# Kernel tuning notes

Measured on AMD Instinct MI355X. Metric: run time of the kernel, lower is better.

Reference implementation:

```python
import jax, jax.numpy as jnp
import numpy as np

EMBEDDING_DIM = 10
CONTEXT_SIZE_1 = 1
CONTEXT_SIZE_2 = 3
VOCAB = 50000
N = 1_000_000
NUM_NUMERIC = 16


def setup_inputs() -> dict:
    key = jax.random.key(0)
    ks = jax.random.split(key, 9)
    text_1 = jax.random.randint(ks[0], (N,), 0, VOCAB)
    text_2 = jax.random.randint(ks[1], (N,), 0, VOCAB)
    numeric_features = jax.random.normal(ks[2], (N, NUM_NUMERIC), dtype=jnp.float32)
    emb_table_1 = jax.random.normal(ks[3], (VOCAB, EMBEDDING_DIM), dtype=jnp.float32)
    emb_table_2 = jax.random.normal(ks[4], (VOCAB, EMBEDDING_DIM), dtype=jnp.float32)
    d_in = 2 * EMBEDDING_DIM + NUM_NUMERIC
    W1 = jax.random.normal(ks[5], (d_in, 128), dtype=jnp.float32) / np.sqrt(d_in)
    b1 = jnp.zeros((128,), dtype=jnp.float32)
    W2 = jax.random.normal(ks[6], (128, 1), dtype=jnp.float32) / np.sqrt(128.0)
    b2 = jnp.zeros((1,), dtype=jnp.float32)
    return {
        "text_1": text_1,
        "text_2": text_2,
        "numeric_features": numeric_features,
        "emb_table_1": emb_table_1,
        "emb_table_2": emb_table_2,
        "W1": W1,
        "b1": b1,
        "W2": W2,
        "b2": b2,
    }


def _contextual_embedding(ids, table, context_size):
    # mean of embeddings over window [i-cs, i+cs], clipped at sequence edges
    n = ids.shape[0]
    emb = table[ids]  # [N, D] gather
    # prefix sums with leading zero row: S[j] = sum(emb[0:j])
    S = jnp.concatenate([jnp.zeros((1, emb.shape[1]), emb.dtype),
                         jnp.cumsum(emb, axis=0)], axis=0)
    pos = jnp.arange(n)
    lo = jnp.maximum(pos - context_size, 0)
    hi = jnp.minimum(pos + context_size + 1, n)
    wsum = S[hi] - S[lo]                       # [N, D]
    count = (hi - lo).astype(emb.dtype)[:, None]
    return wsum / count


def reference(text_1, text_2, numeric_features, emb_table_1, emb_table_2, W1, b1, W2, b2):
    embed_1 = _contextual_embedding(text_1, emb_table_1, CONTEXT_SIZE_1)  # [N, 10]
    embed_2 = _contextual_embedding(text_2, emb_table_2, CONTEXT_SIZE_2)  # [N, 10]
    combined = jnp.concatenate([embed_1, embed_2, numeric_features], axis=1)
    h = jax.nn.relu(combined @ W1 + b1)
    out = h @ W2 + b2
    return jax.nn.sigmoid(out)  # [N, 1]
```

## Files before the change

### kernel.cpp

```cpp
#include <hip/hip_runtime.h>
#include <hip/hip_bf16.h>

#define EMB 10
#define DIN 36
#define HID 128
#define BM  128

typedef __attribute__((ext_vector_type(8))) short short8;
typedef __attribute__((ext_vector_type(4))) float f32x4;

__device__ __forceinline__ short bf16_hi(float v) {
  __hip_bfloat16 h = __float2bfloat16(v);
  return *reinterpret_cast<short*>(&h);
}
__device__ __forceinline__ float bf16_to_f(short s) {
  __hip_bfloat16 h = *reinterpret_cast<__hip_bfloat16*>(&s);
  return __bfloat162float(h);
}

__global__ void prep_kernel(const float* __restrict__ W1, const float* __restrict__ b1,
                            short* __restrict__ Bpack) {
  int b = blockIdx.x;
  int term = b >> 4;
  int ct   = (b >> 1) & 7;
  int ks   = b & 1;
  int l = threadIdx.x;
  int col = ct * 16 + (l & 15);
  int kb  = ks * 32 + (l >> 4) * 8;
  short8 o;
#pragma unroll
  for (int e = 0; e < 8; ++e) {
    int k = kb + e;
    float v = 0.0f;
    if (k < DIN)       v = W1[k * HID + col];
    else if (k == DIN) v = b1[col];
    short hb = bf16_hi(v);
    o[e] = (term == 0) ? hb : bf16_hi(v - bf16_to_f(hb));
  }
  *(short8*)(Bpack + (size_t)(((term * 8 + ct) * 2 + ks) * 64 + l) * 8) = o;
}

__global__ __launch_bounds__(256, 3)
void fused_kernel(const int* __restrict__ t1, const int* __restrict__ t2,
                  const float* __restrict__ numf,
                  const float* __restrict__ tab1, const float* __restrict__ tab2,
                  const short* __restrict__ Bpack,
                  const float* __restrict__ W2, const float* __restrict__ b2,
                  float* __restrict__ out, int N) {
  __shared__ float E1[BM + 2][11];
  __shared__ float E2[BM + 6][11];
  __shared__ short Afrag[2][BM / 16][2][64][8];
  __shared__ float W2s[HID];

  const int tid = threadIdx.x;
  const long base = (long)blockIdx.x * BM;
  const long row = base + tid;
  const bool rv = (tid < BM) && (row < (long)N);

  float4 nf0, nf1, nf2, nf3;
  if (rv) {
    const float4* np = (const float4*)(numf + row * 16);
    nf0 = np[0]; nf1 = np[1]; nf2 = np[2]; nf3 = np[3];
  }
  if (tid < BM + 2) {
    long g = base - 1 + tid;
    if (g >= 0 && g < N) {
      const float* src = tab1 + (long)t1[g] * EMB;
#pragma unroll
      for (int i = 0; i < EMB; ++i) E1[tid][i] = src[i];
    }
  }
  {
    int h = tid - (256 - (BM + 6));
    if (h >= 0) {
      long g = base - 3 + h;
      if (g >= 0 && g < N) {
        const float* src = tab2 + (long)t2[g] * EMB;
#pragma unroll
        for (int i = 0; i < EMB; ++i) E2[h][i] = src[i];
      }
    }
  }
  if (tid >= 128) W2s[tid - 128] = W2[tid - 128];
  __syncthreads();

  if (rv) {
    float c[DIN + 1];
    {
      float s[EMB] = {0,0,0,0,0,0,0,0,0,0};
      int cnt = 0;
#pragma unroll
      for (int d = 0; d < 3; ++d) {
        long g = row - 1 + d;
        if (g >= 0 && g < N) {
          int h = tid + d;
#pragma unroll
          for (int i = 0; i < EMB; ++i) s[i] += E1[h][i];
          ++cnt;
        }
      }
      float inv = 1.0f / (float)cnt;
#pragma unroll
      for (int i = 0; i < EMB; ++i) c[i] = s[i] * inv;
    }
    {
      float s[EMB] = {0,0,0,0,0,0,0,0,0,0};
      int cnt = 0;
#pragma unroll
      for (int d = 0; d < 7; ++d) {
        long g = row - 3 + d;
        if (g >= 0 && g < N) {
          int h = tid + d;
#pragma unroll
          for (int i = 0; i < EMB; ++i) s[i] += E2[h][i];
          ++cnt;
        }
      }
      float inv = 1.0f / (float)cnt;
#pragma unroll
      for (int i = 0; i < EMB; ++i) c[EMB + i] = s[i] * inv;
    }
    c[20] = nf0.x; c[21] = nf0.y; c[22] = nf0.z; c[23] = nf0.w;
    c[24] = nf1.x; c[25] = nf1.y; c[26] = nf1.z; c[27] = nf1.w;
    c[28] = nf2.x; c[29] = nf2.y; c[30] = nf2.z; c[31] = nf2.w;
    c[32] = nf3.x; c[33] = nf3.y; c[34] = nf3.z; c[35] = nf3.w;
    c[DIN] = 1.0f;

    const int rt = tid >> 4;
    const int wr = tid & 15;
#pragma unroll
    for (int g = 0; g < 8; ++g) {
      short8 hi8, lo8;
#pragma unroll
      for (int e = 0; e < 8; ++e) {
        int k = g * 8 + e;
        float v = (k <= DIN) ? c[k] : 0.0f;
        short hb = bf16_hi(v);
        hi8[e] = hb;
        lo8[e] = bf16_hi(v - bf16_to_f(hb));
      }
      int ks = g >> 2;
      int lane = (g & 3) * 16 + wr;
      *(short8*)&Afrag[0][rt][ks][lane][0] = hi8;
      *(short8*)&Afrag[1][rt][ks][lane][0] = lo8;
    }
  }
  __syncthreads();

  const int wid = tid >> 6;
  const int l = tid & 63;

  short8 a[2][2][2];
#pragma unroll
  for (int rtl = 0; rtl < 2; ++rtl) {
    int rt = wid * 2 + rtl;
#pragma unroll
    for (int term = 0; term < 2; ++term)
#pragma unroll
      for (int ks = 0; ks < 2; ++ks)
        a[rtl][term][ks] = *(const short8*)&Afrag[term][rt][ks][l][0];
  }

  float part[2][4] = {{0,0,0,0},{0,0,0,0}};
#pragma unroll
  for (int ct = 0; ct < 8; ++ct) {
    short8 bb[2][2];
#pragma unroll
    for (int term = 0; term < 2; ++term)
#pragma unroll
      for (int ks = 0; ks < 2; ++ks)
        bb[term][ks] = *(const short8*)(Bpack +
            (size_t)(((term * 8 + ct) * 2 + ks) * 64 + l) * 8);
    float w2c = W2s[ct * 16 + (l & 15)];
#pragma unroll
    for (int rtl = 0; rtl < 2; ++rtl) {
      f32x4 acc = {0.0f, 0.0f, 0.0f, 0.0f};
#pragma unroll
      for (int ks = 0; ks < 2; ++ks) {
        acc = __builtin_amdgcn_mfma_f32_16x16x32_bf16(a[rtl][0][ks], bb[0][ks], acc, 0, 0, 0);
        acc = __builtin_amdgcn_mfma_f32_16x16x32_bf16(a[rtl][1][ks], bb[0][ks], acc, 0, 0, 0);
        acc = __builtin_amdgcn_mfma_f32_16x16x32_bf16(a[rtl][0][ks], bb[1][ks], acc, 0, 0, 0);
      }
#pragma unroll
      for (int r = 0; r < 4; ++r) {
        float hv = fmaxf(acc[r], 0.0f);
        part[rtl][r] += hv * w2c;
      }
    }
  }
#pragma unroll
  for (int off = 1; off < 16; off <<= 1) {
#pragma unroll
    for (int rtl = 0; rtl < 2; ++rtl)
#pragma unroll
      for (int r = 0; r < 4; ++r)
        part[rtl][r] += __shfl_xor(part[rtl][r], off, 64);
  }
  if ((l & 15) < 4) {
    float b2v = b2[0];
#pragma unroll
    for (int rtl = 0; rtl < 2; ++rtl) {
      int rt = wid * 2 + rtl;
      long grow = base + rt * 16 + (l >> 4) * 4 + (l & 15);
      if (grow < N) {
        float x = part[rtl][l & 15] + b2v;
        out[grow] = 1.0f / (1.0f + expf(-x));
      }
    }
  }
}

extern "C" void kernel_launch(void* const* d_in, const int* in_sizes, int n_in,
                              void* d_out, int out_size, void* d_ws, size_t ws_size,
                              hipStream_t stream) {
  const int*   t1   = (const int*)d_in[0];
  const int*   t2   = (const int*)d_in[1];
  const float* numf = (const float*)d_in[2];
  const float* tab1 = (const float*)d_in[3];
  const float* tab2 = (const float*)d_in[4];
  const float* W1   = (const float*)d_in[5];
  const float* b1   = (const float*)d_in[6];
  const float* W2   = (const float*)d_in[7];
  const float* b2   = (const float*)d_in[8];
  float* out = (float*)d_out;
  const int N = in_sizes[0];
  short* Bpack = (short*)d_ws;

  hipLaunchKernelGGL(prep_kernel, dim3(32), dim3(64), 0, stream, W1, b1, Bpack);
  int nblk = (N + BM - 1) / BM;
  hipLaunchKernelGGL(fused_kernel, dim3(nblk), dim3(256), 0, stream,
                     t1, t2, numf, tab1, tab2, Bpack, W2, b2, out, N);
}
```

Before: 191.2 us.

## Stage fp32 features in LDS and split to bf16 per MFMA lane

```diff
diff --git a/kernel.cpp b/kernel.cpp
--- a/kernel.cpp
+++ b/kernel.cpp
@@ -40,7 +40,7 @@
   *(short8*)(Bpack + (size_t)(((term * 8 + ct) * 2 + ks) * 64 + l) * 8) = o;
 }
 
-__global__ __launch_bounds__(256, 3)
+__global__ __launch_bounds__(256, 5)
 void fused_kernel(const int* __restrict__ t1, const int* __restrict__ t2,
                   const float* __restrict__ numf,
                   const float* __restrict__ tab1, const float* __restrict__ tab2,
@@ -49,7 +49,7 @@
                   float* __restrict__ out, int N) {
   __shared__ float E1[BM + 2][11];
   __shared__ float E2[BM + 6][11];
-  __shared__ short Afrag[2][BM / 16][2][64][8];
+  __shared__ float Cs[BM][38];
   __shared__ float W2s[HID];
 
   const int tid = threadIdx.x;
@@ -65,9 +65,12 @@
   if (tid < BM + 2) {
     long g = base - 1 + tid;
     if (g >= 0 && g < N) {
-      const float* src = tab1 + (long)t1[g] * EMB;
-#pragma unroll
-      for (int i = 0; i < EMB; ++i) E1[tid][i] = src[i];
+      const float2* src = (const float2*)(tab1 + (long)t1[g] * EMB);
+#pragma unroll
+      for (int i = 0; i < 5; ++i) {
+        float2 v = src[i];
+        E1[tid][2 * i] = v.x; E1[tid][2 * i + 1] = v.y;
+      }
     }
   }
   {
@@ -75,9 +78,12 @@
     if (h >= 0) {
       long g = base - 3 + h;
       if (g >= 0 && g < N) {
-        const float* src = tab2 + (long)t2[g] * EMB;
-#pragma unroll
-        for (int i = 0; i < EMB; ++i) E2[h][i] = src[i];
+        const float2* src = (const float2*)(tab2 + (long)t2[g] * EMB);
+#pragma unroll
+        for (int i = 0; i < 5; ++i) {
+          float2 v = src[i];
+          E2[h][2 * i] = v.x; E2[h][2 * i + 1] = v.y;
+        }
       }
     }
   }
@@ -126,39 +132,54 @@
     c[32] = nf3.x; c[33] = nf3.y; c[34] = nf3.z; c[35] = nf3.w;
     c[DIN] = 1.0f;
 
-    const int rt = tid >> 4;
-    const int wr = tid & 15;
-#pragma unroll
-    for (int g = 0; g < 8; ++g) {
-      short8 hi8, lo8;
-#pragma unroll
-      for (int e = 0; e < 8; ++e) {
-        int k = g * 8 + e;
-        float v = (k <= DIN) ? c[k] : 0.0f;
-        short hb = bf16_hi(v);
-        hi8[e] = hb;
-        lo8[e] = bf16_hi(v - bf16_to_f(hb));
-      }
-      int ks = g >> 2;
-      int lane = (g & 3) * 16 + wr;
-      *(short8*)&Afrag[0][rt][ks][lane][0] = hi8;
-      *(short8*)&Afrag[1][rt][ks][lane][0] = lo8;
-    }
+#pragma unroll
+    for (int k = 0; k <= DIN; ++k) Cs[tid][k] = c[k];
+    Cs[tid][37] = 0.0f;
   }
   __syncthreads();
 
   const int wid = tid >> 6;
   const int l = tid & 63;
-
-  short8 a[2][2][2];
+  const int arow = l & 15;
+  const int kg = l >> 4;
+
+  short8 aHi[2][2], aLo[2][2];
 #pragma unroll
   for (int rtl = 0; rtl < 2; ++rtl) {
-    int rt = wid * 2 + rtl;
-#pragma unroll
-    for (int term = 0; term < 2; ++term)
-#pragma unroll
-      for (int ks = 0; ks < 2; ++ks)
-        a[rtl][term][ks] = *(const short8*)&Afrag[term][rt][ks][l][0];
+    const int r = (wid * 2 + rtl) * 16 + arow;
+    const float* crow = &Cs[r][0];
+    {
+      float v[8];
+#pragma unroll
+      for (int i = 0; i < 4; ++i) {
+        float2 t = *(const float2*)(crow + kg * 8 + 2 * i);
+        v[2 * i] = t.x; v[2 * i + 1] = t.y;
+      }
+#pragma unroll
+      for (int e = 0; e < 8; ++e) {
+        short hb = bf16_hi(v[e]);
+        aHi[rtl][0][e] = hb;
+        aLo[rtl][0][e] = bf16_hi(v[e] - bf16_to_f(hb));
+      }
+    }
+    if (kg == 0) {
+      float v[8];
+#pragma unroll
+      for (int i = 0; i < 3; ++i) {
+        float2 t = *(const float2*)(crow + 32 + 2 * i);
+        v[2 * i] = t.x; v[2 * i + 1] = t.y;
+      }
+      v[6] = 0.0f; v[7] = 0.0f;
+#pragma unroll
+      for (int e = 0; e < 8; ++e) {
+        short hb = bf16_hi(v[e]);
+        aHi[rtl][1][e] = hb;
+        aLo[rtl][1][e] = bf16_hi(v[e] - bf16_to_f(hb));
+      }
+    } else {
+#pragma unroll
+      for (int e = 0; e < 8; ++e) { aHi[rtl][1][e] = 0; aLo[rtl][1][e] = 0; }
+    }
   }
 
   float part[2][4] = {{0,0,0,0},{0,0,0,0}};
@@ -177,9 +198,9 @@
       f32x4 acc = {0.0f, 0.0f, 0.0f, 0.0f};
 #pragma unroll
       for (int ks = 0; ks < 2; ++ks) {
-        acc = __builtin_amdgcn_mfma_f32_16x16x32_bf16(a[rtl][0][ks], bb[0][ks], acc, 0, 0, 0);
-        acc = __builtin_amdgcn_mfma_f32_16x16x32_bf16(a[rtl][1][ks], bb[0][ks], acc, 0, 0, 0);
-        acc = __builtin_amdgcn_mfma_f32_16x16x32_bf16(a[rtl][0][ks], bb[1][ks], acc, 0, 0, 0);
+        acc = __builtin_amdgcn_mfma_f32_16x16x32_bf16(aHi[rtl][ks], bb[0][ks], acc, 0, 0, 0);
+        acc = __builtin_amdgcn_mfma_f32_16x16x32_bf16(aLo[rtl][ks], bb[0][ks], acc, 0, 0, 0);
+        acc = __builtin_amdgcn_mfma_f32_16x16x32_bf16(aHi[rtl][ks], bb[1][ks], acc, 0, 0, 0);
       }
 #pragma unroll
       for (int r = 0; r < 4; ++r) {
```

Result: slower. 299.7 us (+56.7%).
